# Kernel optimization log

Hardware: AMD Instinct MI355X
Metric: run time of the kernel (lower is better)

Reference implementation:

```python
import jax, jax.numpy as jnp
import numpy as np

D = 1024  # input_dim


def setup_inputs() -> dict:
    key = jax.random.key(0)
    ks = jax.random.split(key, 7)
    s = 1.0 / np.sqrt(D)
    x = jax.random.normal(ks[0], (4, 2048, D), dtype=jnp.float32)
    Wq = jax.random.uniform(ks[1], (D, D), jnp.float32, -s, s)
    bq = jax.random.uniform(ks[2], (D,), jnp.float32, -s, s)
    Wk = jax.random.uniform(ks[3], (D, D), jnp.float32, -s, s)
    bk = jax.random.uniform(ks[4], (D,), jnp.float32, -s, s)
    Wv = jax.random.uniform(ks[5], (D, D), jnp.float32, -s, s)
    bv = jax.random.uniform(ks[6], (D,), jnp.float32, -s, s)
    return {"x": x, "Wq": Wq, "bq": bq, "Wk": Wk, "bk": bk, "Wv": Wv, "bv": bv}


def reference(x, Wq, bq, Wk, bk, Wv, bv):
    # nn.Linear: x @ W.T + b
    q = jnp.einsum('bsd,ed->bse', x, Wq) + bq
    k = jnp.einsum('bsd,ed->bse', x, Wk) + bk
    v = jnp.einsum('bsd,ed->bse', x, Wv) + bv
    scale = 1.0 / jnp.sqrt(jnp.asarray(x.shape[-1], x.dtype))
    scores = jnp.einsum('bqe,bke->bqk', q, k) * scale  # [B,S,S]
    weights = jax.nn.softmax(scores, axis=-1)
    return jnp.einsum('bqk,bke->bqe', weights, v)
```

## Files before the change

kernel.cpp:

```cpp
#include <hip/hip_runtime.h>
#include <stdint.h>


typedef float f32x4 __attribute__((ext_vector_type(4)));
typedef short s16x8 __attribute__((ext_vector_type(8)));

__device__ __forceinline__ uint16_t f2bf(float f) {
    uint32_t u = __float_as_uint(f);
    u += 0x7fffu + ((u >> 16) & 1u);
    return (uint16_t)(u >> 16);
}

#define GLOAD16(gp, lp)                                                  \
    __builtin_amdgcn_global_load_lds(                                    \
        (const __attribute__((address_space(1))) uint32_t*)(gp),         \
        (__attribute__((address_space(3))) uint32_t*)(lp), 16, 0, 0)

__device__ __forceinline__ int xcd_swz(int b, int nwg) {
    return (b & 7) * (nwg >> 3) + (b >> 3);
}

__device__ __forceinline__ void gemm_core(
    uint16_t* __restrict__ As, uint16_t* __restrict__ Bs,
    const uint16_t* __restrict__ Ag, const int lda,
    const uint16_t* __restrict__ Bg, const int ldb,
    const int NT, f32x4 (&acc)[4][4])
{
    const int t = threadIdx.x;
    const int wave = t >> 6, lane = t & 63;
    const int wm = (wave >> 1) * 64, wn = (wave & 1) * 64;
    const int lr = lane & 15, hi = lane >> 4, lr7 = lane & 7;

    uint32_t offA[4], offB[4];
#pragma unroll
    for (int p = 0; p < 4; ++p) {
        const int cs = p * 256 + t;
        const int rr = cs >> 3;
        const int kc = ((cs & 7) ^ (rr & 7)) * 8;
        offA[p] = (uint32_t)((rr * lda + kc) * 2);
        offB[p] = (uint32_t)((rr * ldb + kc) * 2);
    }
    const int lws = wave * 512;

    for (int it = 0; it < NT; ++it) {
#pragma unroll
        for (int p = 0; p < 4; ++p) {
            GLOAD16((const uint8_t*)Ag + offA[p], As + p * 2048 + lws);
            offA[p] += 128;
        }
#pragma unroll
        for (int p = 0; p < 4; ++p) {
            GLOAD16((const uint8_t*)Bg + offB[p], Bs + p * 2048 + lws);
            offB[p] += 128;
        }
        __syncthreads();
#pragma unroll
        for (int kk = 0; kk < 2; ++kk) {
            const int lka = ((kk * 4 + hi) ^ lr7) * 8;
            s16x8 a[4], b[4];
#pragma unroll
            for (int i = 0; i < 4; ++i)
                a[i] = *(const s16x8*)(As + (wm + i * 16 + lr) * 64 + lka);
#pragma unroll
            for (int j = 0; j < 4; ++j)
                b[j] = *(const s16x8*)(Bs + (wn + j * 16 + lr) * 64 + lka);
#pragma unroll
            for (int i = 0; i < 4; ++i)
#pragma unroll
                for (int j = 0; j < 4; ++j)
                    acc[i][j] = __builtin_amdgcn_mfma_f32_16x16x32_bf16(
                        a[i], b[j], acc[i][j], 0, 0, 0);
        }
        __syncthreads();
    }
}

__global__ __launch_bounds__(256, 4) void proj_all(
    const uint16_t* __restrict__ xb, const uint16_t* __restrict__ wqb,
    const uint16_t* __restrict__ wkb, const uint16_t* __restrict__ wvb,
    const float* __restrict__ bq, const float* __restrict__ bk,
    const float* __restrict__ bv,
    uint16_t* __restrict__ qb, uint16_t* __restrict__ kb,
    uint16_t* __restrict__ vtb)
{
    __shared__ __attribute__((aligned(16))) uint16_t As[128 * 64];
    __shared__ __attribute__((aligned(16))) uint16_t Bs[128 * 64];

    const int id = xcd_swz(blockIdx.x, 1536);
    const int t = threadIdx.x;
    const int wave = t >> 6, lane = t & 63;
    const int wm = (wave >> 1) * 64, wn = (wave & 1) * 64;
    const int lr = lane & 15, hi = lane >> 4;

    f32x4 acc[4][4] = {};

    if (id < 1024) {
        const int mat = id >> 9;
        const long long row0 = (long long)((id >> 3) & 63) * 128;
        const long long col0 = (long long)(id & 7) * 128;
        const uint16_t* W = mat ? wkb : wqb;
        gemm_core(As, Bs, xb + row0 * 1024, 1024, W + col0 * 1024, 1024, 16, acc);

        const float* bias = mat ? bk : bq;
        uint16_t* out = mat ? kb : qb;
        const float scale = mat ? 1.0f : 0.03125f;
#pragma unroll
        for (int i = 0; i < 4; ++i)
#pragma unroll
            for (int rr = 0; rr < 4; ++rr) {
                const long long row = row0 + wm + i * 16 + hi * 4 + rr;
#pragma unroll
                for (int j = 0; j < 4; ++j) {
                    const long long col = col0 + wn + j * 16 + lr;
                    out[row * 1024 + col] = f2bf((acc[i][j][rr] + bias[col]) * scale);
                }
            }
    } else {
        const int vid = id - 1024;
        const long long row0 = (long long)(vid & 7) * 128;
        const long long col0 = (long long)(vid >> 3) * 128;
        gemm_core(As, Bs, wvb + row0 * 1024, 1024, xb + col0 * 1024, 1024, 16, acc);
#pragma unroll
        for (int i = 0; i < 4; ++i)
#pragma unroll
            for (int rr = 0; rr < 4; ++rr) {
                const long long row = row0 + wm + i * 16 + hi * 4 + rr;
                const float bb = bv[row];
#pragma unroll
                for (int j = 0; j < 4; ++j) {
                    const long long col = col0 + wn + j * 16 + lr;
                    vtb[row * 8192 + col] = f2bf(acc[i][j][rr] + bb);
                }
            }
    }
}

__global__ __launch_bounds__(256, 4) void gemm_exp(
    const uint16_t* __restrict__ Q, const uint16_t* __restrict__ Km,
    uint16_t* __restrict__ P, float* __restrict__ sums)
{
    __shared__ __attribute__((aligned(16))) uint16_t As[128 * 64];
    __shared__ __attribute__((aligned(16))) uint16_t Bs[128 * 64];

    const int id = xcd_swz(blockIdx.x, 1024);
    const int z = id >> 8;
    const int rem = id & 255;
    const long long row0 = (long long)(rem & 15) * 128;
    const long long col0 = (long long)(rem >> 4) * 128;

    const uint16_t* Ab = Q  + (long long)z * 2048 * 1024 + row0 * 1024;
    const uint16_t* Bb = Km + (long long)z * 2048 * 1024 + col0 * 1024;
    uint16_t* Cb = P + (long long)z * 2048 * 2048;
    float* ax = sums + (long long)z * 2048;

    f32x4 acc[4][4] = {};
    gemm_core(As, Bs, Ab, 1024, Bb, 1024, 16, acc);

    const int t = threadIdx.x;
    const int wave = t >> 6, lane = t & 63;
    const int wm = (wave >> 1) * 64, wn = (wave & 1) * 64;
    const int lr = lane & 15, hi = lane >> 4;
#pragma unroll
    for (int i = 0; i < 4; ++i)
#pragma unroll
        for (int rr = 0; rr < 4; ++rr) {
            const long long row = row0 + wm + i * 16 + hi * 4 + rr;
            float s = 0.f;
#pragma unroll
            for (int j = 0; j < 4; ++j) {
                const long long col = col0 + wn + j * 16 + lr;
                const float v = __expf(acc[i][j][rr]);
                Cb[row * 2048 + col] = f2bf(v);
                s += v;
            }
            s += __shfl_xor(s, 1);
            s += __shfl_xor(s, 2);
            s += __shfl_xor(s, 4);
            s += __shfl_xor(s, 8);
            if (lr == 0) atomicAdd(&ax[row], s);
        }
}

__global__ __launch_bounds__(256, 4) void gemm_pv(
    const uint16_t* __restrict__ P, const uint16_t* __restrict__ Vt,
    float* __restrict__ Out, const float* __restrict__ sums)
{
    __shared__ __attribute__((aligned(16))) uint16_t As[128 * 64];
    __shared__ __attribute__((aligned(16))) uint16_t Bs[128 * 64];

    const int id = xcd_swz(blockIdx.x, 512);
    const int z = id >> 7;
    const int rem = id & 127;
    const long long row0 = (long long)(rem & 15) * 128;
    const long long col0 = (long long)(rem >> 4) * 128;

    const uint16_t* Ab = P + (long long)z * 2048 * 2048 + row0 * 2048;
    const uint16_t* Bb = Vt + col0 * 8192 + (long long)z * 2048;
    float* Cb = Out + (long long)z * 2048 * 1024;
    const float* ax = sums + (long long)z * 2048;

    f32x4 acc[4][4] = {};
    gemm_core(As, Bs, Ab, 2048, Bb, 8192, 32, acc);

    const int t = threadIdx.x;
    const int wave = t >> 6, lane = t & 63;
    const int wm = (wave >> 1) * 64, wn = (wave & 1) * 64;
    const int lr = lane & 15, hi = lane >> 4;
#pragma unroll
    for (int i = 0; i < 4; ++i)
#pragma unroll
        for (int rr = 0; rr < 4; ++rr) {
            const long long row = row0 + wm + i * 16 + hi * 4 + rr;
            const float linv = __builtin_amdgcn_rcpf(ax[row]);
#pragma unroll
            for (int j = 0; j < 4; ++j) {
                const long long col = col0 + wn + j * 16 + lr;
                Cb[row * 1024 + col] = acc[i][j][rr] * linv;
            }
        }
}

__global__ void cast_all(const float* __restrict__ x, const float* __restrict__ Wq,
                         const float* __restrict__ Wk, const float* __restrict__ Wv,
                         uint16_t* __restrict__ xb, uint16_t* __restrict__ wqb,
                         uint16_t* __restrict__ wkb, uint16_t* __restrict__ wvb,
                         float* __restrict__ sums) {
    const int b = blockIdx.x;
    const float* in;
    uint16_t* out;
    int i;
    if (b < 8192)       { in = x;  out = xb;  i = b * 256 + threadIdx.x; }
    else if (b < 9216)  { in = Wq; out = wqb; i = (b - 8192) * 256 + threadIdx.x; }
    else if (b < 10240) { in = Wk; out = wkb; i = (b - 9216) * 256 + threadIdx.x; }
    else if (b < 11264) { in = Wv; out = wvb; i = (b - 10240) * 256 + threadIdx.x; }
    else {
        int j = (b - 11264) * 256 + threadIdx.x;
        ((float4*)sums)[j] = make_float4(0.f, 0.f, 0.f, 0.f);
        return;
    }
    float4 v = ((const float4*)in)[i];
    ushort4 o = make_ushort4(f2bf(v.x), f2bf(v.y), f2bf(v.z), f2bf(v.w));
    ((ushort4*)out)[i] = o;
}

extern "C" void kernel_launch(void* const* d_in, const int* in_sizes, int n_in,
                              void* d_out, int out_size, void* d_ws, size_t ws_size,
                              hipStream_t stream) {
    const float* x  = (const float*)d_in[0];
    const float* Wq = (const float*)d_in[1];
    const float* bq = (const float*)d_in[2];
    const float* Wk = (const float*)d_in[3];
    const float* bk = (const float*)d_in[4];
    const float* Wv = (const float*)d_in[5];
    const float* bv = (const float*)d_in[6];

    uint8_t* w = (uint8_t*)d_ws;
    uint16_t* xb  = (uint16_t*)w; w += (size_t)8192 * 1024 * 2;
    uint16_t* wqb = (uint16_t*)w; w += (size_t)1024 * 1024 * 2;
    uint16_t* wkb = (uint16_t*)w; w += (size_t)1024 * 1024 * 2;
    uint16_t* wvb = (uint16_t*)w; w += (size_t)1024 * 1024 * 2;
    uint16_t* qb  = (uint16_t*)w; w += (size_t)8192 * 1024 * 2;
    uint16_t* kb  = (uint16_t*)w; w += (size_t)8192 * 1024 * 2;
    uint16_t* vtb = (uint16_t*)w; w += (size_t)8192 * 1024 * 2;
    uint16_t* pb  = (uint16_t*)w; w += (size_t)4 * 2048 * 2048 * 2;
    float*    sums = (float*)w;  w += (size_t)8192 * 4;

    cast_all<<<dim3(11272), dim3(256), 0, stream>>>(x, Wq, Wk, Wv,
                                                    xb, wqb, wkb, wvb, sums);
    proj_all<<<dim3(1536), dim3(256), 0, stream>>>(xb, wqb, wkb, wvb,
                                                   bq, bk, bv, qb, kb, vtb);
    gemm_exp<<<dim3(1024), dim3(256), 0, stream>>>(qb, kb, pb, sums);
    gemm_pv<<<dim3(512), dim3(256), 0, stream>>>(pb, vtb, (float*)d_out, sums);
}
```

Baseline: 221.2 us.

## Fold Q and K projections into a precomputed Wk^T Wq bilinear form

Rewrites the attention scores as x·(Wq^T Wk)·x^T plus rank-one bias corrections, precomputing the 1024x1024 product matrix and bias vectors inside the cast kernel. The projection kernel then computes only one x·M GEMM plus V instead of separate Q and K GEMMs, and the score kernel adds per-row and per-column bias terms before exp. This removes one large projection GEMM. It adds a low-parallelism 64-block GEMM in the cast stage, an extra memset, and bf16 rounding of the fused matrix, which could affect accuracy.

```diff
diff --git a/kernel.cpp b/kernel.cpp
--- a/kernel.cpp
+++ b/kernel.cpp
@@ -9,6 +9,10 @@
     uint32_t u = __float_as_uint(f);
     u += 0x7fffu + ((u >> 16) & 1u);
     return (uint16_t)(u >> 16);
+}
+
+__device__ __forceinline__ float bf2f(short v) {
+    return __uint_as_float(((uint32_t)(uint16_t)v) << 16);
 }
 
 #define GLOAD16(gp, lp)                                                  \
@@ -75,35 +79,196 @@
     }
 }
 
-__global__ __launch_bounds__(256, 4) void proj_all(
-    const uint16_t* __restrict__ xb, const uint16_t* __restrict__ wqb,
-    const uint16_t* __restrict__ wkb, const uint16_t* __restrict__ wvb,
-    const float* __restrict__ bq, const float* __restrict__ bk,
-    const float* __restrict__ bv,
-    uint16_t* __restrict__ qb, uint16_t* __restrict__ kb,
-    uint16_t* __restrict__ vtb)
+__global__ void cast_all(const float* __restrict__ x, const float* __restrict__ Wq,
+                         const float* __restrict__ Wk, const float* __restrict__ Wv,
+                         const float* __restrict__ bq, const float* __restrict__ bk,
+                         uint16_t* __restrict__ xb, uint16_t* __restrict__ wvb,
+                         uint16_t* __restrict__ mtb, float* __restrict__ w2,
+                         float* __restrict__ w3, float* __restrict__ c4,
+                         float* __restrict__ sums)
 {
     __shared__ __attribute__((aligned(16))) uint16_t As[128 * 64];
     __shared__ __attribute__((aligned(16))) uint16_t Bs[128 * 64];
-
-    const int id = xcd_swz(blockIdx.x, 1536);
+    const int b = blockIdx.x;
+    const int t = threadIdx.x;
+
+    if (b < 64) {
+        const int rowblk = b >> 3, colblk = b & 7;
+        const int wave = t >> 6, lane = t & 63;
+        const int wm = (wave >> 1) * 64, wn = (wave & 1) * 64;
+        const int lr = lane & 15, hi = lane >> 4, lr7 = lane & 7;
+        const int quad = t & 31, ep0 = t >> 5;
+        f32x4 acc[4][4] = {};
+        for (int e0 = 0; e0 < 1024; e0 += 64) {
+#pragma unroll
+            for (int p = 0; p < 4; ++p) {
+                const int e = (ep0 + p * 8) * 2;
+                const int dq = quad * 4;
+                const float* ka = Wk + (long long)(e0 + e) * 1024 + rowblk * 128 + dq;
+                const float* qa = Wq + (long long)(e0 + e) * 1024 + colblk * 128 + dq;
+                float4 a0 = *(const float4*)ka;
+                float4 a1 = *(const float4*)(ka + 1024);
+                float4 b0 = *(const float4*)qa;
+                float4 b1 = *(const float4*)(qa + 1024);
+                const float* a0p = (const float*)&a0;
+                const float* a1p = (const float*)&a1;
+                const float* b0p = (const float*)&b0;
+                const float* b1p = (const float*)&b1;
+#pragma unroll
+                for (int m = 0; m < 4; ++m) {
+                    const int d = dq + m;
+                    const int idx = d * 64 + (((e >> 3) ^ (d & 7)) * 8) + (e & 7);
+                    *(uint32_t*)(As + idx) =
+                        (uint32_t)f2bf(a0p[m]) | ((uint32_t)f2bf(a1p[m]) << 16);
+                    *(uint32_t*)(Bs + idx) =
+                        (uint32_t)f2bf(b0p[m]) | ((uint32_t)f2bf(b1p[m]) << 16);
+                }
+            }
+            __syncthreads();
+#pragma unroll
+            for (int kk = 0; kk < 2; ++kk) {
+                const int lka = ((kk * 4 + hi) ^ lr7) * 8;
+                s16x8 a[4], bb[4];
+#pragma unroll
+                for (int i = 0; i < 4; ++i)
+                    a[i] = *(const s16x8*)(As + (wm + i * 16 + lr) * 64 + lka);
+#pragma unroll
+                for (int j = 0; j < 4; ++j)
+                    bb[j] = *(const s16x8*)(Bs + (wn + j * 16 + lr) * 64 + lka);
+#pragma unroll
+                for (int i = 0; i < 4; ++i)
+#pragma unroll
+                    for (int j = 0; j < 4; ++j)
+                        acc[i][j] = __builtin_amdgcn_mfma_f32_16x16x32_bf16(
+                            a[i], bb[j], acc[i][j], 0, 0, 0);
+            }
+            __syncthreads();
+        }
+        const int row0 = rowblk * 128, col0 = colblk * 128;
+#pragma unroll
+        for (int i = 0; i < 4; ++i)
+#pragma unroll
+            for (int rr = 0; rr < 4; ++rr) {
+                const int row = row0 + wm + i * 16 + hi * 4 + rr;
+#pragma unroll
+                for (int j = 0; j < 4; ++j) {
+                    const int col = col0 + wn + j * 16 + lr;
+                    mtb[row * 1024 + col] = f2bf(acc[i][j][rr] * 0.03125f);
+                }
+            }
+        return;
+    }
+    if (b < 8256) {
+        const int i = (b - 64) * 256 + t;
+        float4 v = ((const float4*)x)[i];
+        ((ushort4*)xb)[i] = make_ushort4(f2bf(v.x), f2bf(v.y), f2bf(v.z), f2bf(v.w));
+        return;
+    }
+    if (b < 8384) {
+        const int blk = b - 8256;
+        float4 a = make_float4(0.f, 0.f, 0.f, 0.f);
+#pragma unroll
+        for (int r = 0; r < 8; ++r) {
+            const int e = blk * 8 + r;
+            const float s = bk[e];
+            float4 v = ((const float4*)(Wq + (long long)e * 1024))[t];
+            a.x += s * v.x; a.y += s * v.y; a.z += s * v.z; a.w += s * v.w;
+        }
+        const int d = t * 4;
+        atomicAdd(&w2[d + 0], a.x * 0.03125f);
+        atomicAdd(&w2[d + 1], a.y * 0.03125f);
+        atomicAdd(&w2[d + 2], a.z * 0.03125f);
+        atomicAdd(&w2[d + 3], a.w * 0.03125f);
+        return;
+    }
+    if (b < 8512) {
+        const int blk = b - 8384;
+        float4 a = make_float4(0.f, 0.f, 0.f, 0.f);
+#pragma unroll
+        for (int r = 0; r < 8; ++r) {
+            const int e = blk * 8 + r;
+            const float s = bq[e];
+            float4 v = ((const float4*)(Wk + (long long)e * 1024))[t];
+            a.x += s * v.x; a.y += s * v.y; a.z += s * v.z; a.w += s * v.w;
+        }
+        const int d = t * 4;
+        atomicAdd(&w3[d + 0], a.x * 0.03125f);
+        atomicAdd(&w3[d + 1], a.y * 0.03125f);
+        atomicAdd(&w3[d + 2], a.z * 0.03125f);
+        atomicAdd(&w3[d + 3], a.w * 0.03125f);
+        return;
+    }
+    if (b < 9536) {
+        const int i = (b - 8512) * 256 + t;
+        float4 v = ((const float4*)Wv)[i];
+        ((ushort4*)wvb)[i] = make_ushort4(f2bf(v.x), f2bf(v.y), f2bf(v.z), f2bf(v.w));
+        return;
+    }
+    if (b < 9544) {
+        const int j = (b - 9536) * 256 + t;
+        ((float4*)sums)[j] = make_float4(0.f, 0.f, 0.f, 0.f);
+        return;
+    }
+    {
+        float4 a = ((const float4*)bq)[t];
+        float4 bb = ((const float4*)bk)[t];
+        float s = a.x * bb.x + a.y * bb.y + a.z * bb.z + a.w * bb.w;
+        s += __shfl_xor(s, 1);  s += __shfl_xor(s, 2);  s += __shfl_xor(s, 4);
+        s += __shfl_xor(s, 8);  s += __shfl_xor(s, 16); s += __shfl_xor(s, 32);
+        float* red = (float*)As;
+        if ((t & 63) == 0) red[t >> 6] = s;
+        __syncthreads();
+        if (t == 0) *c4 = (red[0] + red[1] + red[2] + red[3]) * 0.03125f;
+    }
+}
+
+__global__ __launch_bounds__(256, 4) void proj_all(
+    const uint16_t* __restrict__ xb, const uint16_t* __restrict__ mtb,
+    const uint16_t* __restrict__ wvb, const float* __restrict__ bv,
+    const float* __restrict__ w2, const float* __restrict__ w3,
+    uint16_t* __restrict__ tb, uint16_t* __restrict__ vtb,
+    float* __restrict__ qv, float* __restrict__ kv)
+{
+    __shared__ __attribute__((aligned(16))) uint16_t As[128 * 64];
+    __shared__ __attribute__((aligned(16))) uint16_t Bs[128 * 64];
+
+    const int id = xcd_swz(blockIdx.x, 1152);
     const int t = threadIdx.x;
     const int wave = t >> 6, lane = t & 63;
+
+    if (id >= 1024) {
+        const int dj = id - 1024;
+        const float* wvec = (dj < 64) ? w2 : w3;
+        float* outv = (dj < 64) ? qv : kv;
+        const int base = (dj & 63) * 128 + wave * 32;
+        float wreg[16];
+#pragma unroll
+        for (int m = 0; m < 16; ++m) wreg[m] = wvec[lane * 16 + m];
+        for (int rr = 0; rr < 32; ++rr) {
+            const int row = base + rr;
+            const s16x8* xp = (const s16x8*)(xb + (long long)row * 1024 + lane * 16);
+            const s16x8 v0 = xp[0], v1 = xp[1];
+            float s = 0.f;
+#pragma unroll
+            for (int m = 0; m < 8; ++m) {
+                s += bf2f(v0[m]) * wreg[m];
+                s += bf2f(v1[m]) * wreg[8 + m];
+            }
+            s += __shfl_xor(s, 1);  s += __shfl_xor(s, 2);  s += __shfl_xor(s, 4);
+            s += __shfl_xor(s, 8);  s += __shfl_xor(s, 16); s += __shfl_xor(s, 32);
+            if (lane == 0) outv[row] = s;
+        }
+        return;
+    }
+
     const int wm = (wave >> 1) * 64, wn = (wave & 1) * 64;
     const int lr = lane & 15, hi = lane >> 4;
-
     f32x4 acc[4][4] = {};
 
-    if (id < 1024) {
-        const int mat = id >> 9;
-        const long long row0 = (long long)((id >> 3) & 63) * 128;
+    if (id < 512) {
+        const long long row0 = (long long)(id >> 3) * 128;
         const long long col0 = (long long)(id & 7) * 128;
-        const uint16_t* W = mat ? wkb : wqb;
-        gemm_core(As, Bs, xb + row0 * 1024, 1024, W + col0 * 1024, 1024, 16, acc);
-
-        const float* bias = mat ? bk : bq;
-        uint16_t* out = mat ? kb : qb;
-        const float scale = mat ? 1.0f : 0.03125f;
+        gemm_core(As, Bs, xb + row0 * 1024, 1024, mtb + col0 * 1024, 1024, 16, acc);
 #pragma unroll
         for (int i = 0; i < 4; ++i)
 #pragma unroll
@@ -112,11 +277,11 @@
 #pragma unroll
                 for (int j = 0; j < 4; ++j) {
                     const long long col = col0 + wn + j * 16 + lr;
-                    out[row * 1024 + col] = f2bf((acc[i][j][rr] + bias[col]) * scale);
+                    tb[row * 1024 + col] = f2bf(acc[i][j][rr]);
                 }
             }
     } else {
-        const int vid = id - 1024;
+        const int vid = id - 512;
         const long long row0 = (long long)(vid & 7) * 128;
         const long long col0 = (long long)(vid >> 3) * 128;
         gemm_core(As, Bs, wvb + row0 * 1024, 1024, xb + col0 * 1024, 1024, 16, acc);
@@ -136,8 +301,10 @@
 }
 
 __global__ __launch_bounds__(256, 4) void gemm_exp(
-    const uint16_t* __restrict__ Q, const uint16_t* __restrict__ Km,
-    uint16_t* __restrict__ P, float* __restrict__ sums)
+    const uint16_t* __restrict__ Tm, const uint16_t* __restrict__ X,
+    uint16_t* __restrict__ P, float* __restrict__ sums,
+    const float* __restrict__ qv, const float* __restrict__ kv,
+    const float* __restrict__ c4p)
 {
     __shared__ __attribute__((aligned(16))) uint16_t As[128 * 64];
     __shared__ __attribute__((aligned(16))) uint16_t Bs[128 * 64];
@@ -148,8 +315,8 @@
     const long long row0 = (long long)(rem & 15) * 128;
     const long long col0 = (long long)(rem >> 4) * 128;
 
-    const uint16_t* Ab = Q  + (long long)z * 2048 * 1024 + row0 * 1024;
-    const uint16_t* Bb = Km + (long long)z * 2048 * 1024 + col0 * 1024;
+    const uint16_t* Ab = Tm + (long long)z * 2048 * 1024 + row0 * 1024;
+    const uint16_t* Bb = X  + (long long)z * 2048 * 1024 + col0 * 1024;
     uint16_t* Cb = P + (long long)z * 2048 * 2048;
     float* ax = sums + (long long)z * 2048;
 
@@ -160,16 +327,26 @@
     const int wave = t >> 6, lane = t & 63;
     const int wm = (wave >> 1) * 64, wn = (wave & 1) * 64;
     const int lr = lane & 15, hi = lane >> 4;
+
+    const float c4v = *c4p;
+    const float* qvz = qv + z * 2048;
+    const float* kvz = kv + z * 2048;
+    float kc[4];
+#pragma unroll
+    for (int j = 0; j < 4; ++j)
+        kc[j] = kvz[col0 + wn + j * 16 + lr] + c4v;
+
 #pragma unroll
     for (int i = 0; i < 4; ++i)
 #pragma unroll
         for (int rr = 0; rr < 4; ++rr) {
             const long long row = row0 + wm + i * 16 + hi * 4 + rr;
+            const float qr = qvz[row];
             float s = 0.f;
 #pragma unroll
             for (int j = 0; j < 4; ++j) {
                 const long long col = col0 + wn + j * 16 + lr;
-                const float v = __expf(acc[i][j][rr]);
+                const float v = __expf(acc[i][j][rr] + qr + kc[j]);
                 Cb[row * 2048 + col] = f2bf(v);
                 s += v;
             }
@@ -218,29 +395,6 @@
                 Cb[row * 1024 + col] = acc[i][j][rr] * linv;
             }
         }
-}
-
-__global__ void cast_all(const float* __restrict__ x, const float* __restrict__ Wq,
-                         const float* __restrict__ Wk, const float* __restrict__ Wv,
-                         uint16_t* __restrict__ xb, uint16_t* __restrict__ wqb,
-                         uint16_t* __restrict__ wkb, uint16_t* __restrict__ wvb,
-                         float* __restrict__ sums) {
-    const int b = blockIdx.x;
-    const float* in;
-    uint16_t* out;
-    int i;
-    if (b < 8192)       { in = x;  out = xb;  i = b * 256 + threadIdx.x; }
-    else if (b < 9216)  { in = Wq; out = wqb; i = (b - 8192) * 256 + threadIdx.x; }
-    else if (b < 10240) { in = Wk; out = wkb; i = (b - 9216) * 256 + threadIdx.x; }
-    else if (b < 11264) { in = Wv; out = wvb; i = (b - 10240) * 256 + threadIdx.x; }
-    else {
-        int j = (b - 11264) * 256 + threadIdx.x;
-        ((float4*)sums)[j] = make_float4(0.f, 0.f, 0.f, 0.f);
-        return;
-    }
-    float4 v = ((const float4*)in)[i];
-    ushort4 o = make_ushort4(f2bf(v.x), f2bf(v.y), f2bf(v.z), f2bf(v.w));
-    ((ushort4*)out)[i] = o;
 }
 
 extern "C" void kernel_launch(void* const* d_in, const int* in_sizes, int n_in,
@@ -256,19 +410,26 @@
 
     uint8_t* w = (uint8_t*)d_ws;
     uint16_t* xb  = (uint16_t*)w; w += (size_t)8192 * 1024 * 2;
-    uint16_t* wqb = (uint16_t*)w; w += (size_t)1024 * 1024 * 2;
-    uint16_t* wkb = (uint16_t*)w; w += (size_t)1024 * 1024 * 2;
+    uint16_t* mtb = (uint16_t*)w; w += (size_t)1024 * 1024 * 2;
+    uint8_t*  aux = w;            w += (size_t)2 * 1024 * 1024;
     uint16_t* wvb = (uint16_t*)w; w += (size_t)1024 * 1024 * 2;
-    uint16_t* qb  = (uint16_t*)w; w += (size_t)8192 * 1024 * 2;
-    uint16_t* kb  = (uint16_t*)w; w += (size_t)8192 * 1024 * 2;
+    uint16_t* tb  = (uint16_t*)w; w += (size_t)8192 * 1024 * 2;
     uint16_t* vtb = (uint16_t*)w; w += (size_t)8192 * 1024 * 2;
     uint16_t* pb  = (uint16_t*)w; w += (size_t)4 * 2048 * 2048 * 2;
-    float*    sums = (float*)w;  w += (size_t)8192 * 4;
-
-    cast_all<<<dim3(11272), dim3(256), 0, stream>>>(x, Wq, Wk, Wv,
-                                                    xb, wqb, wkb, wvb, sums);
-    proj_all<<<dim3(1536), dim3(256), 0, stream>>>(xb, wqb, wkb, wvb,
-                                                   bq, bk, bv, qb, kb, vtb);
-    gemm_exp<<<dim3(1024), dim3(256), 0, stream>>>(qb, kb, pb, sums);
+    float*    sums = (float*)w;   w += (size_t)8192 * 4;
+
+    float* w2 = (float*)(aux);
+    float* w3 = (float*)(aux + 4096);
+    float* c4 = (float*)(aux + 8192);
+    float* qv = (float*)(aux + 16384);
+    float* kv = (float*)(aux + 16384 + 32768);
+
+    hipMemsetAsync(aux, 0, 8192 + 256, stream);
+
+    cast_all<<<dim3(9545), dim3(256), 0, stream>>>(x, Wq, Wk, Wv, bq, bk,
+                                                   xb, wvb, mtb, w2, w3, c4, sums);
+    proj_all<<<dim3(1152), dim3(256), 0, stream>>>(xb, mtb, wvb, bv, w2, w3,
+                                                   tb, vtb, qv, kv);
+    gemm_exp<<<dim3(1024), dim3(256), 0, stream>>>(tb, xb, pb, sums, qv, kv, c4);
     gemm_pv<<<dim3(512), dim3(256), 0, stream>>>(pb, vtb, (float*)d_out, sums);
 }
```

New measurement: 281.3 us. 1.27x slower.
